# Performance work log

Hardware: AMD Instinct MI355X
Metric: run time of the kernel (lower is better)

Reference implementation:

```python
import jax, jax.numpy as jnp
import numpy as np

B, T, I, E, K, J = 4, 4096, 512, 16, 1024, 512

def setup_inputs() -> dict:
    key = jax.random.key(0)
    k1, k2, k3 = jax.random.split(key, 3)
    X = jax.random.normal(k1, (B, T, I), dtype=jnp.float32)
    ind = jax.random.randint(k2, (B, E, K), 0, T, dtype=jnp.int64)
    W = jax.random.normal(k3, (E, I, J), dtype=jnp.float32)
    return {"X": X, "ind": ind, "W": W}

def reference(X, ind, W):
    # X: [B,T,I], ind: [B,E,K] indices into T (per batch), W: [E,I,J]
    b, t, i = X.shape
    offset = (jnp.arange(b, dtype=ind.dtype) * t)[:, None, None]  # [B,1,1]
    X_flat = X.reshape(b * t, i)
    gathered = X_flat[ind + offset]              # [B,E,K,I]
    Y = jnp.einsum('beki,eij->bekj', gathered, W)  # [B,E,K,J]
    return Y
```

## Files before the change

kernel.cpp:

```cpp
#include <hip/hip_runtime.h>

#define B_ 4
#define T_ 4096
#define I_ 512
#define E_ 16
#define K_ 1024
#define J_ 512

typedef unsigned short u16;
typedef unsigned int u32;
typedef __attribute__((ext_vector_type(4))) float floatx4;
typedef __attribute__((ext_vector_type(8))) short short8;
typedef __attribute__((ext_vector_type(4))) u16 u16x4;
typedef __attribute__((ext_vector_type(8))) u16 u16x8;

__device__ __forceinline__ u16 f2bf(float f) {
  unsigned int u = __float_as_uint(f);
  u += 0x7FFFu + ((u >> 16) & 1u);
  return (u16)(u >> 16);
}

__device__ __forceinline__ void gload16(const u16* g, u16* l) {
  __builtin_amdgcn_global_load_lds(
      (const __attribute__((address_space(1))) unsigned int*)(g),
      (__attribute__((address_space(3))) unsigned int*)(l),
      16, 0, 0);
}

__global__ __launch_bounds__(256) void prep(const float* __restrict__ X,
                                            const float* __restrict__ W,
                                            u16* __restrict__ Xb,
                                            u16* __restrict__ Wt) {
  const int tid = threadIdx.x;
  const int blk = blockIdx.x;
  if (blk < 1024) {
    __shared__ u16 tile[64][65];
    const int e  = blk >> 6;
    const int bi = (blk >> 3) & 7;
    const int bj = blk & 7;
    const int i0 = bi * 64, j0 = bj * 64;
#pragma unroll
    for (int p = 0; p < 4; ++p) {
      int r = p * 16 + (tid >> 4);
      int c = (tid & 15) * 4;
      floatx4 v = *(const floatx4*)(W + ((size_t)(e * I_ + i0 + r)) * J_ + j0 + c);
      tile[r][c + 0] = f2bf(v[0]);
      tile[r][c + 1] = f2bf(v[1]);
      tile[r][c + 2] = f2bf(v[2]);
      tile[r][c + 3] = f2bf(v[3]);
    }
    __syncthreads();
#pragma unroll
    for (int p = 0; p < 2; ++p) {
      int j = p * 32 + (tid >> 3);
      int ch = tid & 7;
      u16x8 o;
#pragma unroll
      for (int s = 0; s < 8; ++s) o[s] = tile[ch * 8 + s][j];
      *(u16x8*)(Wt + ((size_t)(e * J_ + j0 + j)) * I_ + i0 + ch * 8) = o;
    }
  } else {
    const int n4 = B_ * T_ * I_ / 4;
    int i = (blk - 1024) * 256 + tid;
    const int stride = 2048 * 256;
    for (; i < n4; i += stride) {
      floatx4 v = ((const floatx4*)X)[i];
      u16x4 o;
      o[0] = f2bf(v[0]); o[1] = f2bf(v[1]); o[2] = f2bf(v[2]); o[3] = f2bf(v[3]);
      ((u16x4*)Xb)[i] = o;
    }
  }
}

__global__ __launch_bounds__(256, 2) void gemm_gather(
    const u16* __restrict__ Xb, const u16* __restrict__ Wt,
    const int* __restrict__ ind, float* __restrict__ Y) {
  __shared__ alignas(16) u16 Asf[2][256 * 64];

  const int tid = threadIdx.x;
  const int blk = ((int)blockIdx.x & 7) * 128 + ((int)blockIdx.x >> 3);
  const int m_t = blk & 3;
  const int n_t = (blk >> 2) & 3;
  const int be  = blk >> 4;
  const int e = be & 15;
  const int b = be >> 4;

  const int lane = tid & 63;
  const int wave = tid >> 6;

  const int lr = lane >> 3;
  const int cg = (lane & 7) ^ lr;

  u32 aoff[8];
#pragma unroll
  for (int q = 0; q < 8; ++q) {
    const int r = wave * 64 + q * 8 + lr;
    const int t = ind[be * K_ + m_t * 256 + r];
    aoff[q] = (u32)(b * T_ + t) * I_ + cg * 8;
  }

  const int wj = (wave & 1) * 64;
  const int wk = (wave >> 1) * 128;
  const int ml = lane & 15;
  const int quad = lane >> 4;

  const u16* __restrict__ wbase =
      Wt + ((size_t)(e * J_ + n_t * 128 + wj + ml)) * I_ + quad * 8;

  floatx4 acc[4][8] = {};
  short8 wfA[8], wfB[8];

#pragma unroll
  for (int i = 0; i < 4; ++i) {
    wfA[i]     = *(const short8*)(wbase + i * 16 * I_);
    wfA[4 + i] = *(const short8*)(wbase + i * 16 * I_ + 32);
  }
  {
    u16* ald = &Asf[0][wave * 4096];
#pragma unroll
    for (int q = 0; q < 8; ++q) gload16(Xb + aoff[q], ald + q * 512);
  }
  asm volatile("s_waitcnt vmcnt(0)" ::: "memory");
  __builtin_amdgcn_s_barrier();

#define GSTEP(IT, CURBUF, WCUR, WNXT)                                          \
  {                                                                            \
    constexpr int kk = (IT) * 64;                                              \
    if ((IT) < 7) {                                                            \
      u16* ald = &Asf[(CURBUF) ^ 1][wave * 4096];                              \
      _Pragma("unroll")                                                        \
      for (int q = 0; q < 8; ++q)                                              \
        gload16(Xb + aoff[q] + kk + 64, ald + q * 512);                        \
      _Pragma("unroll")                                                        \
      for (int i = 0; i < 4; ++i) {                                            \
        WNXT[i]     = *(const short8*)(wbase + i * 16 * I_ + kk + 64);         \
        WNXT[4 + i] = *(const short8*)(wbase + i * 16 * I_ + 32 + kk + 64);    \
      }                                                                        \
    }                                                                          \
    _Pragma("unroll")                                                          \
    for (int s = 0; s < 2; ++s) {                                              \
      const int c = s * 4 + quad;                                              \
      _Pragma("unroll")                                                        \
      for (int ik = 0; ik < 8; ++ik) {                                         \
        const int kr = wk + ik * 16 + ml;                                      \
        const short8 xf =                                                      \
            *(const short8*)&Asf[CURBUF][kr * 64 + ((c ^ (kr & 7)) * 8)];      \
        _Pragma("unroll")                                                      \
        for (int iw = 0; iw < 4; ++iw)                                         \
          acc[iw][ik] = __builtin_amdgcn_mfma_f32_16x16x32_bf16(               \
              WCUR[s * 4 + iw], xf, acc[iw][ik], 0, 0, 0);                     \
      }                                                                        \
    }                                                                          \
    asm volatile("s_waitcnt vmcnt(0)" ::: "memory");                           \
    __builtin_amdgcn_s_barrier();                                              \
  }

  GSTEP(0, 0, wfA, wfB)
  GSTEP(1, 1, wfB, wfA)
  GSTEP(2, 0, wfA, wfB)
  GSTEP(3, 1, wfB, wfA)
  GSTEP(4, 0, wfA, wfB)
  GSTEP(5, 1, wfB, wfA)
  GSTEP(6, 0, wfA, wfB)
  GSTEP(7, 1, wfB, wfA)
#undef GSTEP

#pragma unroll
  for (int iw = 0; iw < 4; ++iw) {
    const int j0 = n_t * 128 + wj + iw * 16 + quad * 4;
#pragma unroll
    for (int ik = 0; ik < 8; ++ik) {
      const int k0 = m_t * 256 + wk + ik * 16 + ml;
      *(floatx4*)(Y + ((size_t)(be * K_ + k0)) * J_ + j0) = acc[iw][ik];
    }
  }
}

extern "C" void kernel_launch(void* const* d_in, const int* in_sizes, int n_in,
                              void* d_out, int out_size, void* d_ws,
                              size_t ws_size, hipStream_t stream) {
  const float* X  = (const float*)d_in[0];
  const int* ind  = (const int*)d_in[1];
  const float* W  = (const float*)d_in[2];
  float* Y = (float*)d_out;

  u16* Xb = (u16*)d_ws;
  u16* Wt = (u16*)((char*)d_ws + (size_t)B_ * T_ * I_ * 2);

  prep<<<3072, 256, 0, stream>>>(X, W, Xb, Wt);
  gemm_gather<<<1024, 256, 0, stream>>>(Xb, Wt, ind, Y);
}
```

Before: 222.1 us.

## Stage W tiles through LDS and prefetch gathered X two steps ahead

W fragments were loaded per wave straight from global memory into registers. They are now loaded once per block into a shared LDS tile with a swizzled layout, so waves that share columns reuse the same data. The X double buffer is restructured to prefetch two k-steps ahead using partial vmcnt waits, giving the gathered row loads more latency hiding. The cost is extra LDS (16KB), an extra barrier per step, and exposed single-buffered W loads between steps.

```diff
diff --git a/kernel.cpp b/kernel.cpp
--- a/kernel.cpp
+++ b/kernel.cpp
@@ -76,6 +76,7 @@
     const u16* __restrict__ Xb, const u16* __restrict__ Wt,
     const int* __restrict__ ind, float* __restrict__ Y) {
   __shared__ alignas(16) u16 Asf[2][256 * 64];
+  __shared__ alignas(16) u16 Bsf[128 * 64];
 
   const int tid = threadIdx.x;
   const int blk = ((int)blockIdx.x & 7) * 128 + ((int)blockIdx.x >> 3);
@@ -98,71 +99,72 @@
     const int t = ind[be * K_ + m_t * 256 + r];
     aoff[q] = (u32)(b * T_ + t) * I_ + cg * 8;
   }
+  const u16* bbase =
+      Wt + ((size_t)(e * J_ + n_t * 128 + wave * 32 + lr)) * I_ + cg * 8;
+  u16* bld = Bsf + (wave * 32) * 64;
 
   const int wj = (wave & 1) * 64;
   const int wk = (wave >> 1) * 128;
   const int ml = lane & 15;
   const int quad = lane >> 4;
 
-  const u16* __restrict__ wbase =
-      Wt + ((size_t)(e * J_ + n_t * 128 + wj + ml)) * I_ + quad * 8;
-
   floatx4 acc[4][8] = {};
-  short8 wfA[8], wfB[8];
 
 #pragma unroll
-  for (int i = 0; i < 4; ++i) {
-    wfA[i]     = *(const short8*)(wbase + i * 16 * I_);
-    wfA[4 + i] = *(const short8*)(wbase + i * 16 * I_ + 32);
+  for (int q = 0; q < 4; ++q) gload16(bbase + q * 8 * I_, bld + q * 512);
+  {
+    u16* a0 = &Asf[0][wave * 4096];
+#pragma unroll
+    for (int q = 0; q < 8; ++q) gload16(Xb + aoff[q], a0 + q * 512);
+    u16* a1 = &Asf[1][wave * 4096];
+#pragma unroll
+    for (int q = 0; q < 8; ++q) gload16(Xb + aoff[q] + 64, a1 + q * 512);
   }
-  {
-    u16* ald = &Asf[0][wave * 4096];
-#pragma unroll
-    for (int q = 0; q < 8; ++q) gload16(Xb + aoff[q], ald + q * 512);
-  }
-  asm volatile("s_waitcnt vmcnt(0)" ::: "memory");
+  asm volatile("s_waitcnt vmcnt(8)" ::: "memory");
   __builtin_amdgcn_s_barrier();
 
-#define GSTEP(IT, CURBUF, WCUR, WNXT)                                          \
+#define GSTEP(IT)                                                              \
   {                                                                            \
-    constexpr int kk = (IT) * 64;                                              \
-    if ((IT) < 7) {                                                            \
-      u16* ald = &Asf[(CURBUF) ^ 1][wave * 4096];                              \
-      _Pragma("unroll")                                                        \
-      for (int q = 0; q < 8; ++q)                                              \
-        gload16(Xb + aoff[q] + kk + 64, ald + q * 512);                        \
+    constexpr int cur = (IT) & 1;                                              \
+    _Pragma("unroll")                                                          \
+    for (int s = 0; s < 2; ++s) {                      \
+      const int c = s * 4 + quad;                                              \
+      short8 wf[4];                                                            \
       _Pragma("unroll")                                                        \
       for (int i = 0; i < 4; ++i) {                                            \
-        WNXT[i]     = *(const short8*)(wbase + i * 16 * I_ + kk + 64);         \
-        WNXT[4 + i] = *(const short8*)(wbase + i * 16 * I_ + 32 + kk + 64);    \
+        const int jr = wj + i * 16 + ml;                                       \
+        wf[i] = *(const short8*)&Bsf[jr * 64 + ((c ^ (jr & 7)) * 8)];          \
       }                                                                        \
-    }                                                                          \
-    _Pragma("unroll")                                                          \
-    for (int s = 0; s < 2; ++s) {                                              \
-      const int c = s * 4 + quad;                                              \
       _Pragma("unroll")                                                        \
       for (int ik = 0; ik < 8; ++ik) {                                         \
         const int kr = wk + ik * 16 + ml;                                      \
         const short8 xf =                                                      \
-            *(const short8*)&Asf[CURBUF][kr * 64 + ((c ^ (kr & 7)) * 8)];      \
+            *(const short8*)&Asf[cur][kr * 64 + ((c ^ (kr & 7)) * 8)];         \
         _Pragma("unroll")                                                      \
         for (int iw = 0; iw < 4; ++iw)                                         \
           acc[iw][ik] = __builtin_amdgcn_mfma_f32_16x16x32_bf16(               \
-              WCUR[s * 4 + iw], xf, acc[iw][ik], 0, 0, 0);                     \
+              wf[iw], xf, acc[iw][ik], 0, 0, 0);                               \
       }                                                                        \
     }                                                                          \
-    asm volatile("s_waitcnt vmcnt(0)" ::: "memory");                           \
-    __builtin_amdgcn_s_barrier();                                              \
+    if ((IT) < 7) {                                                            \
+      __builtin_amdgcn_s_barrier();     \
+      _Pragma("unroll")                                                        \
+      for (int q = 0; q < 4; ++q)                          \
+        gload16(bbase + q * 8 * I_ + ((IT) + 1) * 64, bld + q * 512);          \
+      if ((IT) < 6) {                             \
+        u16* ald = &Asf[cur][wave * 4096];                                     \
+        _Pragma("unroll")                                                      \
+        for (int q = 0; q < 8; ++q)                                            \
+          gload16(Xb + aoff[q] + ((IT) + 2) * 64, ald + q * 512);              \
+        asm volatile("s_waitcnt vmcnt(8)" ::: "memory");     \
+      } else {                                                                 \
+        asm volatile("s_waitcnt vmcnt(0)" ::: "memory");       \
+      }                                                                        \
+      __builtin_amdgcn_s_barrier();           \
+    }                                                                          \
   }
 
-  GSTEP(0, 0, wfA, wfB)
-  GSTEP(1, 1, wfB, wfA)
-  GSTEP(2, 0, wfA, wfB)
-  GSTEP(3, 1, wfB, wfA)
-  GSTEP(4, 0, wfA, wfB)
-  GSTEP(5, 1, wfB, wfA)
-  GSTEP(6, 0, wfA, wfB)
-  GSTEP(7, 1, wfB, wfA)
+  GSTEP(0) GSTEP(1) GSTEP(2) GSTEP(3) GSTEP(4) GSTEP(5) GSTEP(6) GSTEP(7)
 #undef GSTEP
 
 #pragma unroll
```

After: 203.5 us. 1.09x faster.
